# Kernel optimization log

Hardware: AMD Instinct MI355X
Metric: run time of the kernel (lower is better)

## Reference

```python
import jax, jax.numpy as jnp
import numpy as np
import math

EPS = 1e-8
B, S, D, H = 8, 4096, 1024, 4
HD = D // H  # head dim


def setup_inputs() -> dict:
    key = jax.random.key(0)
    kx, kz, ki, kf, ko = jax.random.split(key, 5)
    std = math.sqrt(2.0 / (5.0 * HD))  # small_init std per head
    mkw = lambda k: jax.random.normal(k, (H, HD, HD), dtype=jnp.float32) * std
    return {
        "x": jax.random.normal(kx, (B, S, D), dtype=jnp.float32),
        "Wz": mkw(kz),
        "Wi": mkw(ki),
        "Wf": mkw(kf),
        "Wo": mkw(ko),
    }


def _headwise(x, W):
    b, s, d = x.shape
    xh = x.reshape(b, s, H, HD)
    return jnp.einsum("bshi,hoi->bsho", xh, W).reshape(b, s, d)


def _slstm(x, Wz, Wi, Wf, Wo):
    z_all = _headwise(x, Wz)
    i_all = _headwise(x, Wi)
    f_all = _headwise(x, Wf)
    o_all = _headwise(x, Wo)

    def step(carry, gates):
        c, n, m = carry
        zt, it, ft, ot = gates
        z = jnp.tanh(zt)
        o = jax.nn.sigmoid(ot)
        # log(exp(x)) kept explicit for faithfulness to the original stabilization
        log_i = jnp.log(jnp.exp(it))
        log_f = jnpp_log(ft) if False else jnp.log(jnp.exp(ft))
        m_new = jnp.maximum(log_f + m, log_i)
        i_hat = jnp.exp(log_i - m_new)
        f_hat = jnp.exp(log_f + m - m_new)
        c_new = f_hat * c + i_hat * z
        n_new = f_hat * n + i_hat
        h = o * (c_new / (n_new + EPS))
        return (c_new, n_new, m_new), h

    b = x.shape[0]
    zeros = jnp.zeros((b, D), dtype=x.dtype)
    gates = (
        jnp.swapaxes(z_all, 0, 1),  # [S,B,D]
        jnp.swapaxes(i_all, 0, 1),
        jnp.swapaxes(f_all, 0, 1),
        jnp.swapaxes(o_all, 0, 1),
    )
    _, hs = jax.lax.scan(step, (zeros, zeros, zeros), gates)
    return jnp.swapaxes(hs, 0, 1)  # [B,S,D]


def reference(x, Wz, Wi, Wf, Wo):
    return _slstm(x, Wz, Wi, Wf, Wo)
```

## Files before the change

kernel.cpp:

```cpp
#include <hip/hip_runtime.h>
#include <hip/hip_bf16.h>

typedef __attribute__((ext_vector_type(4))) float f32x4;
typedef __attribute__((ext_vector_type(8))) _Float16 f16x8;
typedef __attribute__((ext_vector_type(4))) _Float16 f16x4;

constexpr int KCH = 64;
constexpr int LCH = 64;
constexpr int CH  = 8192;

constexpr size_t G_OFF   = 20971520;
constexpr size_t G_PLANE = 33554432;

__global__ __launch_bounds__(256) void cvt_w(const float* __restrict__ Wz,
                                             const float* __restrict__ Wi,
                                             const float* __restrict__ Wf,
                                             const float* __restrict__ Wo,
                                             _Float16* __restrict__ Whf) {
  int i = blockIdx.x * 256 + threadIdx.x;
  int flat = i << 2;
  int g = flat >> 18;
  int rest = flat & 262143;
  const float* src = (g == 0) ? Wz : (g == 1) ? Wi : (g == 2) ? Wf : Wo;
  f32x4 v = *(const f32x4*)(src + rest);
  f16x4 h;
#pragma unroll
  for (int j = 0; j < 4; ++j) h[j] = (_Float16)v[j];
  *(f16x4*)(Whf + flat) = h;
}

__global__ __launch_bounds__(512, 6)
void gemm_f16(const float* __restrict__ x,
              const _Float16* __restrict__ Whf,
              _Float16* __restrict__ G) {
  extern __shared__ _Float16 sm[];
  _Float16* Af = sm;
  _Float16* Bf = sm + 8192;

  int bid = blockIdx.x;
  int mt = (bid & 7) + ((bid >> 8) << 3);
  int s  = (bid >> 3) & 31;
  int g  = s & 3;
  int dt = s >> 2;
  int r0 = mt << 7;
  int d0 = dt << 7;
  int h  = d0 >> 8;
  int o0 = d0 & 255;

  int tid = threadIdx.x, lane = tid & 63, wid = tid >> 6;
  int wm = wid >> 1, wn = wid & 1;
  int lr = lane & 15, hi2 = lane >> 4;

  const _Float16* wB = Whf + (((size_t)((g << 2) | h)) << 16);

  int arow = tid >> 2;
  int kq   = (tid & 3) << 4;
  const float* xrow = x + (size_t)(r0 + arow) * 1024 + (h << 8) + kq;

  f32x4 acc[2][4] = {};

  for (int kt = 0; kt < 4; ++kt) {
    int k0 = kt << 6;
    {
      const float* xp = xrow + k0;
#pragma unroll
      for (int p = 0; p < 2; ++p) {
        f32x4 v0 = *(const f32x4*)(xp + p * 8);
        f32x4 v1 = *(const f32x4*)(xp + p * 8 + 4);
        f16x8 hv;
        hv[0] = (_Float16)v0.x; hv[1] = (_Float16)v0.y;
        hv[2] = (_Float16)v0.z; hv[3] = (_Float16)v0.w;
        hv[4] = (_Float16)v1.x; hv[5] = (_Float16)v1.y;
        hv[6] = (_Float16)v1.z; hv[7] = (_Float16)v1.w;
        int kc = (kq >> 3) + p;
        int cidx = (arow << 3) + (kc ^ (arow & 7));
        *(f16x8*)(Af + cidx * 8) = hv;
      }
    }
#pragma unroll
    for (int p = 0; p < 2; ++p) {
      int c = (p << 9) + tid;
      int row = c >> 3;
      int kcd = (c & 7) ^ (row & 7);
      const _Float16* srcp = wB + (size_t)(o0 + row) * 256 + k0 + (kcd << 3);
      __builtin_amdgcn_global_load_lds(
          (const __attribute__((address_space(1))) void*)srcp,
          (__attribute__((address_space(3))) void*)(Bf + c * 8), 16, 0, 0);
    }
    __syncthreads();
#pragma unroll
    for (int ks = 0; ks < 2; ++ks) {
      int kcf = (ks << 2) + hi2;
      f16x8 af[2], bf[4];
#pragma unroll
      for (int mf = 0; mf < 2; ++mf) {
        int row = (wm << 5) + (mf << 4) + lr;
        int cidx = (row << 3) + (kcf ^ (row & 7));
        af[mf] = *(const f16x8*)(Af + cidx * 8);
      }
#pragma unroll
      for (int nf = 0; nf < 4; ++nf) {
        int row = (wn << 6) + (nf << 4) + lr;
        int cidx = (row << 3) + (kcf ^ (row & 7));
        bf[nf] = *(const f16x8*)(Bf + cidx * 8);
      }
#pragma unroll
      for (int mf = 0; mf < 2; ++mf)
#pragma unroll
        for (int nf = 0; nf < 4; ++nf)
          acc[mf][nf] = __builtin_amdgcn_mfma_f32_16x16x32_f16(af[mf], bf[nf],
                                                               acc[mf][nf], 0, 0, 0);
    }
    __syncthreads();
  }
  _Float16* Gg = G + (size_t)g * G_PLANE;
#pragma unroll
  for (int mf = 0; mf < 2; ++mf)
#pragma unroll
    for (int nf = 0; nf < 4; ++nf) {
      int d = d0 + (wn << 6) + (nf << 4) + lr;
      int rowb = r0 + (wm << 5) + (mf << 4) + (hi2 << 2);
#pragma unroll
      for (int j = 0; j < 4; ++j)
        Gg[(size_t)(rowb + j) * 1024 + d] = (_Float16)acc[mf][nf][j];
    }
}

__global__ __launch_bounds__(256) void scan_partial_g(const _Float16* __restrict__ G,
                                                      f32x4* __restrict__ summ) {
  __shared__ _Float16 Ls[3 * 16 * 256];
  int kc = blockIdx.x >> 5;
  int cb = blockIdx.x & 31;
  int b = cb >> 2;
  int d0 = (cb & 3) << 8;
  int tid = threadIdx.x;
  size_t base = (size_t)(b * 4096 + kc * LCH) * 1024 + d0;

  f16x8 rbuf[3][2];
#pragma unroll
  for (int p = 0; p < 3; ++p)
#pragma unroll
    for (int lp = 0; lp < 2; ++lp) {
      int li = (lp << 8) + tid;
      int t = li >> 5, dc = (li & 31) << 3;
      rbuf[p][lp] = *(const f16x8*)(G + p * G_PLANE + base + (size_t)t * 1024 + dc);
    }

  float m = -INFINITY, c = 0.f, n = 0.f, sf = 0.f;
  for (int st = 0; st < 4; ++st) {
#pragma unroll
    for (int p = 0; p < 3; ++p)
#pragma unroll
      for (int lp = 0; lp < 2; ++lp) {
        int li = (lp << 8) + tid;
        int t = li >> 5, dc = (li & 31) << 3;
        *(f16x8*)(&Ls[((p << 4) + t << 8) + dc]) = rbuf[p][lp];
      }
    __syncthreads();
    if (st < 3) {
#pragma unroll
      for (int p = 0; p < 3; ++p)
#pragma unroll
        for (int lp = 0; lp < 2; ++lp) {
          int li = (lp << 8) + tid;
          int t = li >> 5, dc = (li & 31) << 3;
          rbuf[p][lp] = *(const f16x8*)(G + p * G_PLANE + base +
                                        (size_t)((st + 1) * 16 + t) * 1024 + dc);
        }
    }
#pragma unroll 4
    for (int t = 0; t < 16; ++t) {
      float zt = (float)Ls[(t << 8) + tid];
      float it = (float)Ls[((16 + t) << 8) + tid];
      float ft = (float)Ls[((32 + t) << 8) + tid];
      float z = tanhf(zt);
      float mn = fmaxf(ft + m, it);
      float ih = __expf(it - mn);
      float fh = __expf(ft + m - mn);
      c = fh * c + ih * z;
      n = fh * n + ih;
      m = mn;
      sf += ft;
    }
    __syncthreads();
  }
  int chan = (b << 10) + d0 + tid;
  summ[(size_t)kc * CH + chan] = f32x4{sf, c, n, m};
}

__global__ __launch_bounds__(256) void scan_apply_g(const _Float16* __restrict__ G,
                                                    const f32x4* __restrict__ states,
                                                    float* __restrict__ out) {
  __shared__ _Float16 Ls[4 * 16 * 256];
  int kc = blockIdx.x >> 5;
  int cb = blockIdx.x & 31;
  int b = cb >> 2;
  int d0 = (cb & 3) << 8;
  int tid = threadIdx.x;
  size_t base = (size_t)(b * 4096 + kc * LCH) * 1024 + d0;
  float* op = out + base + tid;

  f16x8 rbuf[4][2];
#pragma unroll
  for (int p = 0; p < 4; ++p)
#pragma unroll
    for (int lp = 0; lp < 2; ++lp) {
      int li = (lp << 8) + tid;
      int t = li >> 5, dc = (li & 31) << 3;
      rbuf[p][lp] = *(const f16x8*)(G + p * G_PLANE + base + (size_t)t * 1024 + dc);
    }

  int chan = (b << 10) + d0 + tid;
  f32x4 stv = states[(size_t)kc * CH + chan];
  float c = stv.x, n = stv.y, m = stv.z;

  for (int st = 0; st < 4; ++st) {
#pragma unroll
    for (int p = 0; p < 4; ++p)
#pragma unroll
      for (int lp = 0; lp < 2; ++lp) {
        int li = (lp << 8) + tid;
        int t = li >> 5, dc = (li & 31) << 3;
        *(f16x8*)(&Ls[((p << 4) + t << 8) + dc]) = rbuf[p][lp];
      }
    __syncthreads();
    if (st < 3) {
#pragma unroll
      for (int p = 0; p < 4; ++p)
#pragma unroll
        for (int lp = 0; lp < 2; ++lp) {
          int li = (lp << 8) + tid;
          int t = li >> 5, dc = (li & 31) << 3;
          rbuf[p][lp] = *(const f16x8*)(G + p * G_PLANE + base +
                                        (size_t)((st + 1) * 16 + t) * 1024 + dc);
        }
    }
#pragma unroll 4
    for (int t = 0; t < 16; ++t) {
      float zt = (float)Ls[(t << 8) + tid];
      float it = (float)Ls[((16 + t) << 8) + tid];
      float ft = (float)Ls[((32 + t) << 8) + tid];
      float ot = (float)Ls[((48 + t) << 8) + tid];
      float z = tanhf(zt);
      float og = 1.f / (1.f + __expf(-ot));
      float mn = fmaxf(ft + m, it);
      float ih = __expf(it - mn);
      float fh = __expf(ft + m - mn);
      c = fh * c + ih * z;
      n = fh * n + ih;
      m = mn;
      op[(size_t)(st * 16 + t) * 1024] = og * (c / (n + 1e-8f));
    }
    __syncthreads();
  }
}

__global__ __launch_bounds__(256) void scan_combine(const f32x4* __restrict__ summ,
                                                    f32x4* __restrict__ states) {
  int chan = blockIdx.x * 256 + threadIdx.x;
  float c = 0.f, n = 0.f, m = 0.f;
  for (int kc = 0; kc < KCH; ++kc) {
    states[(size_t)kc * CH + chan] = f32x4{c, n, m, 0.f};
    f32x4 sm = summ[(size_t)kc * CH + chan];
    float mn = fmaxf(m + sm.x, sm.w);
    float ea = __expf(m + sm.x - mn);
    float eb = __expf(sm.w - mn);
    c = ea * c + eb * sm.y;
    n = ea * n + eb * sm.z;
    m = mn;
  }
}

extern "C" void kernel_launch(void* const* d_in, const int* in_sizes, int n_in,
                              void* d_out, int out_size, void* d_ws, size_t ws_size,
                              hipStream_t stream) {
  const float* x  = (const float*)d_in[0];
  const float* Wz = (const float*)d_in[1];
  const float* Wi = (const float*)d_in[2];
  const float* Wf = (const float*)d_in[3];
  const float* Wo = (const float*)d_in[4];
  float* out = (float*)d_out;

  char* ws = (char*)d_ws;
  _Float16* Whf = (_Float16*)(ws);
  f32x4* summ   = (f32x4*)(ws + 4194304);
  f32x4* states = (f32x4*)(ws + 12582912);
  _Float16* G   = (_Float16*)(ws + G_OFF);

  cvt_w<<<1024, 256, 0, stream>>>(Wz, Wi, Wf, Wo, Whf);
  gemm_f16<<<8192, 512, 32768, stream>>>(x, Whf, G);
  scan_partial_g<<<2048, 256, 0, stream>>>(G, summ);
  scan_combine<<<32, 256, 0, stream>>>(summ, states);
  scan_apply_g<<<2048, 256, 0, stream>>>(G, states, out);
}
```

Before: 481.8 us.

## Store gate preactivations channel-major so scans read contiguous time runs

The GEMM epilogue now writes gate tensors transposed to [gate][batch*channel][time], packing four fp16 values per store. Each scan thread can then load its own channel's time series with 16-byte vector loads straight into registers, removing the LDS staging and block barriers in the partial scan. The apply kernel stages outputs through LDS to keep coalesced fp32 stores, and tanh, sigmoid and divide use fast-math exp forms. The GEMM's transposed stores hit strided addresses with only 8-byte granularity, and the per-thread loads are strided by 8 KB across lanes, so coalescing now depends on the cache.

```diff
diff --git a/kernel.cpp b/kernel.cpp
--- a/kernel.cpp
+++ b/kernel.cpp
@@ -32,7 +32,7 @@
 __global__ __launch_bounds__(512, 6)
 void gemm_f16(const float* __restrict__ x,
               const _Float16* __restrict__ Whf,
-              _Float16* __restrict__ G) {
+              _Float16* __restrict__ Gt) {
   extern __shared__ _Float16 sm[];
   _Float16* Af = sm;
   _Float16* Bf = sm + 8192;
@@ -113,143 +113,156 @@
     }
     __syncthreads();
   }
-  _Float16* Gg = G + (size_t)g * G_PLANE;
+  int bb = r0 >> 12;
+  int sbase = r0 & 4095;
+  _Float16* Gg = Gt + (size_t)g * G_PLANE;
 #pragma unroll
   for (int mf = 0; mf < 2; ++mf)
 #pragma unroll
     for (int nf = 0; nf < 4; ++nf) {
       int d = d0 + (wn << 6) + (nf << 4) + lr;
-      int rowb = r0 + (wm << 5) + (mf << 4) + (hi2 << 2);
-#pragma unroll
-      for (int j = 0; j < 4; ++j)
-        Gg[(size_t)(rowb + j) * 1024 + d] = (_Float16)acc[mf][nf][j];
-    }
-}
-
-__global__ __launch_bounds__(256) void scan_partial_g(const _Float16* __restrict__ G,
+      int sx = sbase + (wm << 5) + (mf << 4) + (hi2 << 2);
+      f16x4 pk;
+#pragma unroll
+      for (int j = 0; j < 4; ++j) pk[j] = (_Float16)acc[mf][nf][j];
+      *(f16x4*)(Gg + (((size_t)((bb << 10) + d)) << 12) + sx) = pk;
+    }
+}
+
+__global__ __launch_bounds__(256) void scan_partial_g(const _Float16* __restrict__ Gt,
                                                       f32x4* __restrict__ summ) {
-  __shared__ _Float16 Ls[3 * 16 * 256];
   int kc = blockIdx.x >> 5;
   int cb = blockIdx.x & 31;
-  int b = cb >> 2;
-  int d0 = (cb & 3) << 8;
-  int tid = threadIdx.x;
-  size_t base = (size_t)(b * 4096 + kc * LCH) * 1024 + d0;
-
-  f16x8 rbuf[3][2];
-#pragma unroll
-  for (int p = 0; p < 3; ++p)
-#pragma unroll
-    for (int lp = 0; lp < 2; ++lp) {
-      int li = (lp << 8) + tid;
-      int t = li >> 5, dc = (li & 31) << 3;
-      rbuf[p][lp] = *(const f16x8*)(G + p * G_PLANE + base + (size_t)t * 1024 + dc);
-    }
+  int chan = cb * 256 + threadIdx.x;
+  const _Float16* gz = Gt + ((size_t)chan << 12) + kc * LCH;
+  const _Float16* gi = gz + G_PLANE;
+  const _Float16* gf = gz + 2 * G_PLANE;
+
+  f16x8 bzA = *(const f16x8*)(gz),     bzB = *(const f16x8*)(gz + 8);
+  f16x8 biA = *(const f16x8*)(gi),     biB = *(const f16x8*)(gi + 8);
+  f16x8 bfA = *(const f16x8*)(gf),     bfB = *(const f16x8*)(gf + 8);
 
   float m = -INFINITY, c = 0.f, n = 0.f, sf = 0.f;
-  for (int st = 0; st < 4; ++st) {
-#pragma unroll
-    for (int p = 0; p < 3; ++p)
-#pragma unroll
-      for (int lp = 0; lp < 2; ++lp) {
-        int li = (lp << 8) + tid;
-        int t = li >> 5, dc = (li & 31) << 3;
-        *(f16x8*)(&Ls[((p << 4) + t << 8) + dc]) = rbuf[p][lp];
-      }
-    __syncthreads();
-    if (st < 3) {
-#pragma unroll
-      for (int p = 0; p < 3; ++p)
-#pragma unroll
-        for (int lp = 0; lp < 2; ++lp) {
-          int li = (lp << 8) + tid;
-          int t = li >> 5, dc = (li & 31) << 3;
-          rbuf[p][lp] = *(const f16x8*)(G + p * G_PLANE + base +
-                                        (size_t)((st + 1) * 16 + t) * 1024 + dc);
-        }
-    }
-#pragma unroll 4
-    for (int t = 0; t < 16; ++t) {
-      float zt = (float)Ls[(t << 8) + tid];
-      float it = (float)Ls[((16 + t) << 8) + tid];
-      float ft = (float)Ls[((32 + t) << 8) + tid];
-      float z = tanhf(zt);
-      float mn = fmaxf(ft + m, it);
-      float ih = __expf(it - mn);
-      float fh = __expf(ft + m - mn);
-      c = fh * c + ih * z;
-      n = fh * n + ih;
-      m = mn;
-      sf += ft;
-    }
-    __syncthreads();
+#pragma unroll
+  for (int sp = 0; sp < 4; ++sp) {
+    {
+      f16x8 vz = bzA, vi = biA, vf = bfA;
+      if (sp < 3) {
+        bzA = *(const f16x8*)(gz + (sp * 2 + 2) * 8);
+        biA = *(const f16x8*)(gi + (sp * 2 + 2) * 8);
+        bfA = *(const f16x8*)(gf + (sp * 2 + 2) * 8);
+      }
+#pragma unroll
+      for (int j = 0; j < 8; ++j) {
+        float zt = (float)vz[j], it = (float)vi[j], ft = (float)vf[j];
+        float z = 1.f - __fdividef(2.f, __expf(2.f * zt) + 1.f);
+        float mn = fmaxf(ft + m, it);
+        float ih = __expf(it - mn);
+        float fh = __expf(ft + m - mn);
+        c = fh * c + ih * z;
+        n = fh * n + ih;
+        m = mn;
+        sf += ft;
+      }
+    }
+    {
+      f16x8 vz = bzB, vi = biB, vf = bfB;
+      if (sp < 3) {
+        bzB = *(const f16x8*)(gz + (sp * 2 + 3) * 8);
+        biB = *(const f16x8*)(gi + (sp * 2 + 3) * 8);
+        bfB = *(const f16x8*)(gf + (sp * 2 + 3) * 8);
+      }
+#pragma unroll
+      for (int j = 0; j < 8; ++j) {
+        float zt = (float)vz[j], it = (float)vi[j], ft = (float)vf[j];
+        float z = 1.f - __fdividef(2.f, __expf(2.f * zt) + 1.f);
+        float mn = fmaxf(ft + m, it);
+        float ih = __expf(it - mn);
+        float fh = __expf(ft + m - mn);
+        c = fh * c + ih * z;
+        n = fh * n + ih;
+        m = mn;
+        sf += ft;
+      }
+    }
   }
-  int chan = (b << 10) + d0 + tid;
   summ[(size_t)kc * CH + chan] = f32x4{sf, c, n, m};
 }
 
-__global__ __launch_bounds__(256) void scan_apply_g(const _Float16* __restrict__ G,
+__global__ __launch_bounds__(256) void scan_apply_g(const _Float16* __restrict__ Gt,
                                                     const f32x4* __restrict__ states,
                                                     float* __restrict__ out) {
-  __shared__ _Float16 Ls[4 * 16 * 256];
+  __shared__ float Ls[16 * 256];
   int kc = blockIdx.x >> 5;
   int cb = blockIdx.x & 31;
-  int b = cb >> 2;
-  int d0 = (cb & 3) << 8;
-  int tid = threadIdx.x;
-  size_t base = (size_t)(b * 4096 + kc * LCH) * 1024 + d0;
-  float* op = out + base + tid;
-
-  f16x8 rbuf[4][2];
-#pragma unroll
-  for (int p = 0; p < 4; ++p)
-#pragma unroll
-    for (int lp = 0; lp < 2; ++lp) {
-      int li = (lp << 8) + tid;
-      int t = li >> 5, dc = (li & 31) << 3;
-      rbuf[p][lp] = *(const f16x8*)(G + p * G_PLANE + base + (size_t)t * 1024 + dc);
-    }
-
+  int b = cb >> 2, d0 = (cb & 3) << 8;
+  int tid = threadIdx.x, lane = tid & 63, w = tid >> 6;
   int chan = (b << 10) + d0 + tid;
+  const _Float16* gz = Gt + ((size_t)chan << 12) + kc * LCH;
+  const _Float16* gi = gz + G_PLANE;
+  const _Float16* gf = gz + 2 * G_PLANE;
+  const _Float16* go = gz + 3 * G_PLANE;
+  float* ob = out + (size_t)(b * 4096 + kc * LCH) * 1024 + d0;
+
   f32x4 stv = states[(size_t)kc * CH + chan];
   float c = stv.x, n = stv.y, m = stv.z;
 
+  f16x8 bzA = *(const f16x8*)(gz),     bzB = *(const f16x8*)(gz + 8);
+  f16x8 biA = *(const f16x8*)(gi),     biB = *(const f16x8*)(gi + 8);
+  f16x8 bfA = *(const f16x8*)(gf),     bfB = *(const f16x8*)(gf + 8);
+  f16x8 boA = *(const f16x8*)(go),     boB = *(const f16x8*)(go + 8);
+
   for (int st = 0; st < 4; ++st) {
-#pragma unroll
-    for (int p = 0; p < 4; ++p)
-#pragma unroll
-      for (int lp = 0; lp < 2; ++lp) {
-        int li = (lp << 8) + tid;
-        int t = li >> 5, dc = (li & 31) << 3;
-        *(f16x8*)(&Ls[((p << 4) + t << 8) + dc]) = rbuf[p][lp];
-      }
+    {
+      f16x8 vz = bzA, vi = biA, vf = bfA, vo = boA;
+      if (st < 3) {
+        bzA = *(const f16x8*)(gz + (st * 2 + 2) * 8);
+        biA = *(const f16x8*)(gi + (st * 2 + 2) * 8);
+        bfA = *(const f16x8*)(gf + (st * 2 + 2) * 8);
+        boA = *(const f16x8*)(go + (st * 2 + 2) * 8);
+      }
+#pragma unroll
+      for (int j = 0; j < 8; ++j) {
+        float zt = (float)vz[j], it = (float)vi[j], ft = (float)vf[j], ot = (float)vo[j];
+        float z = 1.f - __fdividef(2.f, __expf(2.f * zt) + 1.f);
+        float og = __fdividef(1.f, 1.f + __expf(-ot));
+        float mn = fmaxf(ft + m, it);
+        float ih = __expf(it - mn);
+        float fh = __expf(ft + m - mn);
+        c = fh * c + ih * z;
+        n = fh * n + ih;
+        m = mn;
+        Ls[j * 256 + tid] = og * __fdividef(c, n + 1e-8f);
+      }
+    }
+    {
+      f16x8 vz = bzB, vi = biB, vf = bfB, vo = boB;
+      if (st < 3) {
+        bzB = *(const f16x8*)(gz + (st * 2 + 3) * 8);
+        biB = *(const f16x8*)(gi + (st * 2 + 3) * 8);
+        bfB = *(const f16x8*)(gf + (st * 2 + 3) * 8);
+        boB = *(const f16x8*)(go + (st * 2 + 3) * 8);
+      }
+#pragma unroll
+      for (int j = 0; j < 8; ++j) {
+        float zt = (float)vz[j], it = (float)vi[j], ft = (float)vf[j], ot = (float)vo[j];
+        float z = 1.f - __fdividef(2.f, __expf(2.f * zt) + 1.f);
+        float og = __fdividef(1.f, 1.f + __expf(-ot));
+        float mn = fmaxf(ft + m, it);
+        float ih = __expf(it - mn);
+        float fh = __expf(ft + m - mn);
+        c = fh * c + ih * z;
+        n = fh * n + ih;
+        m = mn;
+        Ls[(8 + j) * 256 + tid] = og * __fdividef(c, n + 1e-8f);
+      }
+    }
     __syncthreads();
-    if (st < 3) {
-#pragma unroll
-      for (int p = 0; p < 4; ++p)
-#pragma unroll
-        for (int lp = 0; lp < 2; ++lp) {
-          int li = (lp << 8) + tid;
-          int t = li >> 5, dc = (li & 31) << 3;
-          rbuf[p][lp] = *(const f16x8*)(G + p * G_PLANE + base +
-                                        (size_t)((st + 1) * 16 + t) * 1024 + dc);
-        }
-    }
-#pragma unroll 4
-    for (int t = 0; t < 16; ++t) {
-      float zt = (float)Ls[(t << 8) + tid];
-      float it = (float)Ls[((16 + t) << 8) + tid];
-      float ft = (float)Ls[((32 + t) << 8) + tid];
-      float ot = (float)Ls[((48 + t) << 8) + tid];
-      float z = tanhf(zt);
-      float og = 1.f / (1.f + __expf(-ot));
-      float mn = fmaxf(ft + m, it);
-      float ih = __expf(it - mn);
-      float fh = __expf(ft + m - mn);
-      c = fh * c + ih * z;
-      n = fh * n + ih;
-      m = mn;
-      op[(size_t)(st * 16 + t) * 1024] = og * (c / (n + 1e-8f));
+#pragma unroll
+    for (int r = 0; r < 4; ++r) {
+      int tt = (w << 2) + r;
+      f32x4 v = *(const f32x4*)&Ls[tt * 256 + (lane << 2)];
+      *(f32x4*)&ob[(size_t)(st * 16 + tt) * 1024 + (lane << 2)] = v;
     }
     __syncthreads();
   }
@@ -259,6 +272,7 @@
                                                     f32x4* __restrict__ states) {
   int chan = blockIdx.x * 256 + threadIdx.x;
   float c = 0.f, n = 0.f, m = 0.f;
+#pragma unroll 4
   for (int kc = 0; kc < KCH; ++kc) {
     states[(size_t)kc * CH + chan] = f32x4{c, n, m, 0.f};
     f32x4 sm = summ[(size_t)kc * CH + chan];
@@ -285,11 +299,11 @@
   _Float16* Whf = (_Float16*)(ws);
   f32x4* summ   = (f32x4*)(ws + 4194304);
   f32x4* states = (f32x4*)(ws + 12582912);
-  _Float16* G   = (_Float16*)(ws + G_OFF);
+  _Float16* Gt  = (_Float16*)(ws + G_OFF);
 
   cvt_w<<<1024, 256, 0, stream>>>(Wz, Wi, Wf, Wo, Whf);
-  gemm_f16<<<8192, 512, 32768, stream>>>(x, Whf, G);
-  scan_partial_g<<<2048, 256, 0, stream>>>(G, summ);
+  gemm_f16<<<8192, 512, 32768, stream>>>(x, Whf, Gt);
+  scan_partial_g<<<2048, 256, 0, stream>>>(Gt, summ);
   scan_combine<<<32, 256, 0, stream>>>(summ, states);
-  scan_apply_g<<<2048, 256, 0, stream>>>(G, states, out);
-}
+  scan_apply_g<<<2048, 256, 0, stream>>>(Gt, states, out);
+}
```

After: 727.7 us. +51.0%, slower.
